# Kernel optimization log

Measured on AMD Instinct MI355X. Metric: run time of the kernel, lower is better.

Reference implementation:

```python
import jax, jax.numpy as jnp
import numpy as np
from jax import lax

# dims: B batch, C=d_model=256, IMG=128, P=4 patch, H=W=32, L=H*W=1024
# D=d_inner=512 (ssm_ratio 2.0), N=d_state=16, R=dt_rank=16, K=4 scan directions
B, C, IMG, P = 2, 256, 128, 4
H = W = IMG // P
L = H * W
D_INNER, N, R, K = 512, 16, 16, 4


def layernorm(x, g, b, eps=1e-5):
    mu = jnp.mean(x, axis=-1, keepdims=True)
    var = jnp.var(x, axis=-1, keepdims=True)
    return (x - mu) * lax.rsqrt(var + eps) * g + b


def setup_inputs() -> dict:
    key = jax.random.key(0)
    ks = jax.random.split(key, 12)
    f = lambda i, shape, s=0.02: jax.random.normal(ks[i], shape, jnp.float32) * s
    A_init = jnp.tile(jnp.arange(1, N + 1, dtype=jnp.float32)[None, None, :], (K, D_INNER, 1))
    return {
        "x": jax.random.normal(ks[0], (B, C, IMG, IMG), jnp.float32),
        "patch_w": f(1, (C, C, P, P)),
        "patch_b": jnp.zeros((C,), jnp.float32),
        "ln_g": jnp.ones((C,), jnp.float32),
        "ln_b": jnp.zeros((C,), jnp.float32),
        "in_w": f(2, (2 * D_INNER, C)),
        "conv_w": f(3, (D_INNER, 1, 3, 3)),
        "conv_b": jnp.zeros((D_INNER,), jnp.float32),
        "xproj_w": f(4, (K, R + 2 * N, D_INNER)),
        "dt_w": f(5, (K, D_INNER, R)),
        "dt_b": f(6, (K, D_INNER), 0.1),
        "A_log": jnp.log(A_init),
        "Ds": jnp.ones((K, D_INNER), jnp.float32),
        "on_g": jnp.ones((D_INNER,), jnp.float32),
        "on_b": jnp.zeros((D_INNER,), jnp.float32),
        "out_w": f(7, (C, D_INNER)),
        "head_w": f(8, (1, C)),
        "head_b": jnp.zeros((1,), jnp.float32),
    }


def _forward(x, patch_w, patch_b, ln_g, ln_b, in_w, conv_w, conv_b, xproj_w,
             dt_w, dt_b, A_log, Ds, on_g, on_b, out_w, head_w, head_b):
    dn = ("NCHW", "OIHW", "NCHW")
    # GRL is identity in forward. Patch embed conv, stride = patch.
    t = lax.conv_general_dilated(x, patch_w, (P, P), "VALID", dimension_numbers=dn)
    t = t + patch_b[None, :, None, None]
    t = jnp.transpose(t, (0, 2, 3, 1))                      # (B,H,W,C)

    # ---- VSS block: t + SS2D(LN(t)) ----
    u = layernorm(t, ln_g, ln_b)
    xz = jnp.einsum("bhwc,ec->bhwe", u, in_w)               # (B,H,W,2D)
    xc, z = jnp.split(xz, 2, axis=-1)
    xc = jnp.transpose(xc, (0, 3, 1, 2))                    # (B,D,H,W)
    xc = lax.conv_general_dilated(xc, conv_w, (1, 1), "SAME",
                                  dimension_numbers=dn, feature_group_count=D_INNER)
    xc = jax.nn.silu(xc + conv_b[None, :, None, None])

    # cross-scan: row-major, col-major, and their reverses -> (B,K,D,L)
    x_hw = xc.reshape(B, D_INNER, L)
    x_wh = jnp.transpose(xc, (0, 1, 3, 2)).reshape(B, D_INNER, L)
    xs = jnp.stack([x_hw, x_wh], axis=1)
    xs = jnp.concatenate([xs, jnp.flip(xs, axis=-1)], axis=1)  # (B,4,D,L)

    x_dbl = jnp.einsum("bkdl,kcd->bkcl", xs, xproj_w)          # (B,K,R+2N,L)
    dts_r = x_dbl[:, :, :R]
    Bs = x_dbl[:, :, R:R + N]                                  # (B,K,N,L)
    Cs = x_dbl[:, :, R + N:]                                   # (B,K,N,L)
    dts = jnp.einsum("bkrl,kdr->bkdl", dts_r, dt_w) + dt_b[None, :, :, None]
    dts = jax.nn.softplus(dts)                                 # (B,K,D,L)

    A = -jnp.exp(A_log)                                        # (K,D,N)
    dA = jnp.exp(dts[:, :, :, None, :] * A[None, :, :, :, None])      # (B,K,D,N,L)
    dBu = (dts * xs)[:, :, :, None, :] * Bs[:, :, None, :, :]         # (B,K,D,N,L)

    dA_t = jnp.moveaxis(dA, -1, 0)        # (L,B,K,D,N)
    dBu_t = jnp.moveaxis(dBu, -1, 0)
    Cs_t = jnp.moveaxis(Cs, -1, 0)        # (L,B,K,N)

    def step(h, inputs):
        dA_i, dBu_i, C_i = inputs
        h = dA_i * h + dBu_i
        y = jnp.einsum("bkdn,bkn->bkd", h, C_i)
        return h, y

    h0 = jnp.zeros((B, K, D_INNER, N), xs.dtype)
    _, ys = lax.scan(step, h0, (dA_t, dBu_t, Cs_t))           # ys: (L,B,K,D)
    ys = jnp.moveaxis(ys, 0, -1)                               # (B,K,D,L)
    ys = ys + Ds[None, :, :, None] * xs

    # cross-merge (invert the 4 scan orders and sum)
    y_rev = jnp.flip(ys[:, 2:], axis=-1)                        # (B,2,D,L)
    y_hw = ys[:, 0] + y_rev[:, 0]
    y_wh = ys[:, 1] + y_rev[:, 1]
    y_wh = jnp.transpose(y_wh.reshape(B, D_INNER, W, H), (0, 1, 3, 2)).reshape(B, D_INNER, L)
    y = (y_hw + y_wh).reshape(B, D_INNER, H, W)
    y = jnp.transpose(y, (0, 2, 3, 1))                          # (B,H,W,D)

    y = layernorm(y, on_g, on_b) * jax.nn.silu(z)
    ss_out = jnp.einsum("bhwd,cd->bhwc", y, out_w)
    t = t + ss_out

    # global average pool + head
    pooled = jnp.mean(t, axis=(1, 2))                           # (B,C)
    return pooled @ head_w.T + head_b


def reference(x, patch_w, patch_b, ln_g, ln_b, in_w, conv_w, conv_b, xproj_w,
              dt_w, dt_b, A_log, Ds, on_g, on_b, out_w, head_w, head_b):
    return _forward(x, patch_w, patch_b, ln_g, ln_b, in_w, conv_w, conv_b, xproj_w,
                    dt_w, dt_b, A_log, Ds, on_g, on_b, out_w, head_w, head_b)
```

## Files before the change

kernel.cpp:

```cpp
#include <hip/hip_runtime.h>
#include <math.h>


typedef __attribute__((ext_vector_type(4))) float f32x4;
typedef __attribute__((ext_vector_type(8))) short bf16x8;

__device__ __forceinline__ ushort bf16_rn(float f) {
  uint u = __float_as_uint(f);
  return (ushort)((u + 0x7fffu + ((u >> 16) & 1u)) >> 16);
}
__device__ __forceinline__ float bf2f(uint us) { return __uint_as_float(us << 16); }
__device__ __forceinline__ uint packbf(float a, float b) {
  return (uint)bf16_rn(a) | ((uint)bf16_rn(b) << 16);
}

__global__ __launch_bounds__(256) void prep_kernel(const float* __restrict__ x,
    ushort* __restrict__ Ap,
    const float* __restrict__ pw, const float* __restrict__ iw,
    const float* __restrict__ ow, const float* __restrict__ xw,
    const float* __restrict__ hw,
    ushort* __restrict__ pwh,
    ushort* __restrict__ iwh, ushort* __restrict__ iwl,
    ushort* __restrict__ xwh, ushort* __restrict__ xwl,
    float* __restrict__ weff) {
  int bid = blockIdx.x;
  int tid = threadIdx.x;
  if (bid < 2048) {
    __shared__ __align__(16) ushort tile[32][136];
    int b = bid >> 10, hh = (bid >> 5) & 31, c0 = (bid & 31) * 8;
    int ci = tid >> 5, ph = (tid >> 3) & 3, w4 = tid & 7;
    const float* src = x + (((long)(b * 256 + c0 + ci) * 128 + 4 * hh + ph) * 128 + 16 * w4);
    #pragma unroll
    for (int j = 0; j < 4; ++j) {
      float4 v = *(const float4*)(src + 4 * j);
      uint2 pk;
      pk.x = packbf(v.x, v.y);
      pk.y = packbf(v.z, v.w);
      *(uint2*)&tile[w4 * 4 + j][ci * 16 + ph * 4] = pk;
    }
    __syncthreads();
    int w = tid >> 3;
    long rowbase = ((long)(b * 1024 + hh * 32 + w)) * 4096 + c0 * 16;
    #pragma unroll
    for (int i = 0; i < 2; ++i) {
      int gr = (tid & 7) + 8 * i;
      *(uint4*)&Ap[rowbase + gr * 8] = *(const uint4*)&tile[w][gr * 8];
    }
  } else {
    int i = (bid - 2048) * 256 + tid;
    if (i < 1048576) {
      pwh[i] = bf16_rn(pw[i]);
      return;
    }
    if (i < 1409024) {
      const float* src; ushort* hi; ushort* lo; int off;
      if (i < 1310720) { src = iw; hi = iwh; lo = iwl; off = i - 1048576; }
      else             { src = xw; hi = xwh; lo = xwl; off = i - 1310720; }
      float f = src[off];
      ushort h = bf16_rn(f);
      hi[off] = h;
      lo[off] = bf16_rn(f - __uint_as_float(((uint)h) << 16));
      return;
    }
    if (i < 1409536) {
      int k = i - 1409024;
      float s = 0.f;
      #pragma unroll 8
      for (int c = 0; c < 256; ++c) s += ow[c * 512 + k] * hw[c];
      weff[k] = s;
    }
  }
}

__global__ __launch_bounds__(512) void mfma_bf(
    const ushort* __restrict__ A, const ushort* __restrict__ Bhi,
    const ushort* __restrict__ Blo, float* __restrict__ Cout, float* __restrict__ C2,
    int M, int N, int K, int kchunk, int mode, int NBM, int NBZ, int uselo)
{
  __shared__ __align__(16) ushort Ah[128 * 64];
  __shared__ __align__(16) ushort Bh[64 * 64];
  __shared__ __align__(16) ushort Bl[64 * 64];
  int tid = threadIdx.x;
  int bid = blockIdx.x;
  int kz = bid % NBZ;
  int n0 = (bid / (NBZ * NBM)) * 64;
  int m0 = ((bid / NBZ) % NBM) * 128;
  int k0 = kz * kchunk;
  int wid = tid >> 6, lane = tid & 63;
  int wm = wid >> 1, wn = wid & 1;
  int lrow = lane & 15, g = lane >> 4;
  f32x4 acc[2][2] = {};
  int nkt = kchunk >> 6;
  for (int kt = 0; kt < nkt; ++kt) {
    int kb = k0 + (kt << 6);
    {
      int gi = tid & 7;
      #pragma unroll
      for (int i = 0; i < 2; ++i) {
        int row = (tid >> 3) + (i << 6);
        uint4 v = *(const uint4*)&A[(long)(m0 + row) * K + kb + gi * 8];
        *(uint4*)&Ah[row * 64 + ((gi ^ (row & 7)) << 3)] = v;
      }
      int row = tid >> 3;
      long off = (long)(n0 + row) * K + kb + gi * 8;
      int la = row * 64 + ((gi ^ (row & 7)) << 3);
      *(uint4*)&Bh[la] = *(const uint4*)&Bhi[off];
      if (uselo) *(uint4*)&Bl[la] = *(const uint4*)&Blo[off];
    }
    __syncthreads();
    #pragma unroll
    for (int kk = 0; kk < 2; ++kk) {
      bf16x8 af[2], bhf[2];
      #pragma unroll
      for (int mi = 0; mi < 2; ++mi) {
        int row = wm * 32 + mi * 16 + lrow;
        af[mi] = *(const bf16x8*)&Ah[row * 64 + ((((kk << 2) + g) ^ (row & 7)) << 3)];
      }
      #pragma unroll
      for (int ni = 0; ni < 2; ++ni) {
        int row = wn * 32 + ni * 16 + lrow;
        int col = (((kk << 2) + g) ^ (row & 7)) << 3;
        bhf[ni] = *(const bf16x8*)&Bh[row * 64 + col];
      }
      #pragma unroll
      for (int mi = 0; mi < 2; ++mi)
        #pragma unroll
        for (int ni = 0; ni < 2; ++ni)
          acc[mi][ni] = __builtin_amdgcn_mfma_f32_16x16x32_bf16(af[mi], bhf[ni], acc[mi][ni], 0, 0, 0);
      if (uselo) {
        #pragma unroll
        for (int ni = 0; ni < 2; ++ni) {
          int row = wn * 32 + ni * 16 + lrow;
          int col = (((kk << 2) + g) ^ (row & 7)) << 3;
          bf16x8 blf = *(const bf16x8*)&Bl[row * 64 + col];
          #pragma unroll
          for (int mi = 0; mi < 2; ++mi)
            acc[mi][ni] = __builtin_amdgcn_mfma_f32_16x16x32_bf16(af[mi], blf, acc[mi][ni], 0, 0, 0);
        }
      }
    }
    __syncthreads();
  }
  int r4 = lane >> 4;
  if (mode == 2) {
    bool xhalf = (n0 < 512);
    ushort* xcb = (ushort*)Cout;
    #pragma unroll
    for (int mi = 0; mi < 2; ++mi)
      #pragma unroll
      for (int ni = 0; ni < 2; ++ni) {
        int n = n0 + wn * 32 + ni * 16 + lrow;
        int mb = m0 + wm * 32 + mi * 16 + r4 * 4;
        int bb = mb >> 10, l = mb & 1023;
        if (xhalf) {
          uint2 o;
          o.x = packbf(acc[mi][ni][0], acc[mi][ni][1]);
          o.y = packbf(acc[mi][ni][2], acc[mi][ni][3]);
          *(uint2*)&xcb[((long)(bb * 512 + n)) * 1024 + l] = o;
        } else {
          #pragma unroll
          for (int r = 0; r < 4; ++r)
            C2[(long)(mb + r) * 512 + (n - 512)] = acc[mi][ni][r];
        }
      }
  } else {
    long zoff = (long)kz * M * N;
    #pragma unroll
    for (int mi = 0; mi < 2; ++mi)
      #pragma unroll
      for (int ni = 0; ni < 2; ++ni) {
        int n = n0 + wn * 32 + ni * 16 + lrow;
        int mb = m0 + wm * 32 + mi * 16 + r4 * 4;
        #pragma unroll
        for (int r = 0; r < 4; ++r)
          Cout[zoff + (long)(mb + r) * N + n] = acc[mi][ni][r];
      }
  }
}

__global__ __launch_bounds__(256) void mfma_x(
    const ushort* __restrict__ A, const ushort* __restrict__ Bhi,
    const ushort* __restrict__ Blo, float* __restrict__ xdbl)
{
  __shared__ __align__(16) ushort Ah[64 * 64];
  __shared__ __align__(16) ushort Bh[48 * 64];
  __shared__ __align__(16) ushort Bl[48 * 64];
  int tid = threadIdx.x;
  int m0 = blockIdx.x * 64;
  int z = blockIdx.y, k = z & 3;
  const ushort* Az = A + (long)z * 524288;
  const ushort* Bhz = Bhi + (long)k * 24576;
  const ushort* Blz = Blo + (long)k * 24576;
  int lane = tid & 63, wv = tid >> 6;
  int lrow = lane & 15, g = lane >> 4;
  f32x4 acc[3] = {};
  for (int kt = 0; kt < 8; ++kt) {
    int kb = kt << 6;
    #pragma unroll
    for (int i = 0; i < 2; ++i) {
      int idx = i * 256 + tid;
      int row = idx >> 3, gi = idx & 7;
      uint4 v = *(const uint4*)&Az[(long)(m0 + row) * 512 + kb + gi * 8];
      *(uint4*)&Ah[row * 64 + ((gi ^ (row & 7)) << 3)] = v;
      if (idx < 384) {
        long off = (long)row * 512 + kb + gi * 8;
        int la = row * 64 + ((gi ^ (row & 7)) << 3);
        *(uint4*)&Bh[la] = *(const uint4*)&Bhz[off];
        *(uint4*)&Bl[la] = *(const uint4*)&Blz[off];
      }
    }
    __syncthreads();
    #pragma unroll
    for (int kk = 0; kk < 2; ++kk) {
      int arow = wv * 16 + lrow;
      bf16x8 af = *(const bf16x8*)&Ah[arow * 64 + ((((kk << 2) + g) ^ (arow & 7)) << 3)];
      #pragma unroll
      for (int ni = 0; ni < 3; ++ni) {
        int brow = ni * 16 + lrow;
        int col = (((kk << 2) + g) ^ (brow & 7)) << 3;
        bf16x8 bh = *(const bf16x8*)&Bh[brow * 64 + col];
        bf16x8 bl = *(const bf16x8*)&Bl[brow * 64 + col];
        acc[ni] = __builtin_amdgcn_mfma_f32_16x16x32_bf16(af, bh, acc[ni], 0, 0, 0);
        acc[ni] = __builtin_amdgcn_mfma_f32_16x16x32_bf16(af, bl, acc[ni], 0, 0, 0);
      }
    }
    __syncthreads();
  }
  float* Cz = xdbl + (long)z * 49152;
  int r4 = lane >> 4;
  #pragma unroll
  for (int ni = 0; ni < 3; ++ni) {
    int n = ni * 16 + lrow;
    int mb = m0 + wv * 16 + r4 * 4;
    #pragma unroll
    for (int r = 0; r < 4; ++r)
      Cz[(long)(mb + r) * 48 + n] = acc[ni][r];
  }
}

__device__ __forceinline__ float blk_sum(float v, float* sm) {
  #pragma unroll
  for (int o = 32; o > 0; o >>= 1) v += __shfl_down(v, o);
  int wid = threadIdx.x >> 6, lane = threadIdx.x & 63;
  __syncthreads();
  if (lane == 0) sm[wid] = v;
  __syncthreads();
  return sm[0] + sm[1] + sm[2] + sm[3];
}
__device__ __forceinline__ void blk_sum2(float& a, float& b, float* sm) {
  #pragma unroll
  for (int o = 32; o > 0; o >>= 1) { a += __shfl_down(a, o); b += __shfl_down(b, o); }
  int wid = threadIdx.x >> 6, lane = threadIdx.x & 63;
  __syncthreads();
  if (lane == 0) { sm[wid * 2] = a; sm[wid * 2 + 1] = b; }
  __syncthreads();
  a = sm[0] + sm[2] + sm[4] + sm[6];
  b = sm[1] + sm[3] + sm[5] + sm[7];
}
__device__ __forceinline__ void blk_sum3(float& a, float& b, float& c, float* sm) {
  #pragma unroll
  for (int o = 32; o > 0; o >>= 1) {
    a += __shfl_down(a, o); b += __shfl_down(b, o); c += __shfl_down(c, o);
  }
  int wid = threadIdx.x >> 6, lane = threadIdx.x & 63;
  __syncthreads();
  if (lane == 0) { sm[wid * 3] = a; sm[wid * 3 + 1] = b; sm[wid * 3 + 2] = c; }
  __syncthreads();
  a = sm[0] + sm[3] + sm[6] + sm[9];
  b = sm[1] + sm[4] + sm[7] + sm[10];
  c = sm[2] + sm[5] + sm[8] + sm[11];
}

__global__ __launch_bounds__(256) void reduce_ln1(const float* __restrict__ P,
    const float* __restrict__ bias, const float* __restrict__ g,
    const float* __restrict__ b, ushort* __restrict__ u,
    const float* __restrict__ hw, float* __restrict__ tpart) {
  __shared__ float sm[12];
  int m = blockIdx.x, c = threadIdx.x;
  float v = bias[c];
  #pragma unroll
  for (int s = 0; s < 4; ++s) v += P[(long)s * 524288 + m * 256 + c];
  float s1 = v, s2 = v * v, s3 = v * hw[c];
  blk_sum3(s1, s2, s3, sm);
  if (c == 0) tpart[m] = s3;
  float mu = s1 * (1.f / 256.f);
  float var = s2 * (1.f / 256.f) - mu * mu;
  float rs = rsqrtf(var + 1e-5f);
  u[(long)m * 256 + c] = bf16_rn((v - mu) * rs * g[c] + b[c]);
}

__global__ __launch_bounds__(256) void head_final(const float* __restrict__ tpart,
    const float* __restrict__ spart, const float* __restrict__ hb,
    float* __restrict__ out) {
  __shared__ float sm[4];
  int b = blockIdx.x, tid = threadIdx.x;
  float s = 0.f;
  #pragma unroll
  for (int j = 0; j < 4; ++j) {
    int m = b * 1024 + tid * 4 + j;
    s += tpart[m] + spart[m];
  }
  float tot = blk_sum(s, sm);
  if (tid == 0) out[b] = tot * (1.f / 1024.f) + hb[0];
}

__global__ __launch_bounds__(256) void dwbuild(const ushort* __restrict__ xc,
    const float* __restrict__ cw, const float* __restrict__ cb,
    ushort* __restrict__ xsTb) {
  __shared__ float pl[3][32][33];
  __shared__ ushort tile[32][34];
  int h = blockIdx.x;
  int d0 = blockIdx.y * 32;
  int z = blockIdx.z;
  int b = z >> 2, k = z & 3;
  int tid = threadIdx.x;
  int dd = tid >> 3, w4 = (tid & 7) * 4;
  #pragma unroll
  for (int r = 0; r < 3; ++r) {
    int hh = h - 1 + r;
    float4 vv = make_float4(0.f, 0.f, 0.f, 0.f);
    if (hh >= 0 && hh < 32) {
      uint2 v = *(const uint2*)&xc[((long)(b * 512 + d0 + dd)) * 1024 + hh * 32 + w4];
      vv.x = bf2f(v.x & 0xffff); vv.y = bf2f(v.x >> 16);
      vv.z = bf2f(v.y & 0xffff); vv.w = bf2f(v.y >> 16);
    }
    pl[r][dd][w4] = vv.x; pl[r][dd][w4 + 1] = vv.y;
    pl[r][dd][w4 + 2] = vv.z; pl[r][dd][w4 + 3] = vv.w;
  }
  float w9[9];
  #pragma unroll
  for (int i = 0; i < 9; ++i) w9[i] = cw[(d0 + dd) * 9 + i];
  float bias = cb[d0 + dd];
  __syncthreads();
  #pragma unroll
  for (int j = 0; j < 4; ++j) {
    int w = w4 + j;
    float acc = 0.f;
    #pragma unroll
    for (int r = 0; r < 3; ++r) {
      if (w > 0)  acc += w9[r * 3 + 0] * pl[r][dd][w - 1];
      acc += w9[r * 3 + 1] * pl[r][dd][w];
      if (w < 31) acc += w9[r * 3 + 2] * pl[r][dd][w + 1];
    }
    acc += bias;
    tile[dd][w] = bf16_rn(acc / (1.f + __expf(-acc)));
  }
  __syncthreads();
  int a = tid >> 5, q = tid & 31;
  #pragma unroll
  for (int i = 0; i < 4; ++i) {
    int w = a + i * 8;
    int r;
    if (k == 0) r = h * 32 + w;
    else if (k == 1) r = w * 32 + h;
    else if (k == 2) r = 1023 - (h * 32 + w);
    else r = 1023 - (w * 32 + h);
    xsTb[((long)z * 1024 + r) * 512 + d0 + q] = tile[q][w];
  }
}

template<bool FINAL>
__global__ __launch_bounds__(128) void scan_chunk6(
    const float* __restrict__ xdbl, ushort* xsb,
    const float* __restrict__ dtw, const float* __restrict__ dtb,
    const float* __restrict__ A_log, const float* __restrict__ Ds,
    float* __restrict__ dsum, float* __restrict__ hpb)
{
  __shared__ float sdt[32][64];
  __shared__ float sxv[16][64];
  __shared__ float sy[16][64];
  __shared__ float sBC[32][32];
  float (*sR)[16] = (float(*)[16])sy;
  int tid = threadIdx.x;
  int dl = tid >> 1, ng = tid & 1;
  int d0 = blockIdx.x * 64;
  int d = d0 + dl;
  int c = blockIdx.y;
  int z = blockIdx.z;
  int k = z & 3;
  long baseD = (long)z * 524288;
  int l0 = c * 32;
  const float* xdz = xdbl + (long)z * 49152 + (long)l0 * 48;
  #pragma unroll
  for (int i = 0; i < 2; ++i) {
    int idx = i * 128 + tid;
    int l = idx >> 3, q = idx & 7;
    *(float4*)&sBC[l][q * 4] = *(const float4*)(xdz + l * 48 + 16 + q * 4);
  }
  {
    int l = tid >> 2, q = tid & 3;
    *(float4*)&sR[l][q * 4] = *(const float4*)(xdz + l * 48 + q * 4);
  }
  float a[8], h[8];
  #pragma unroll
  for (int j = 0; j < 8; ++j) {
    a[j] = -__expf(A_log[((long)k * 512 + d) * 16 + ng * 8 + j]);
    h[j] = 0.f;
  }
  float4 wr0 = *(const float4*)(dtw + ((long)k * 512 + d) * 16);
  float4 wr1 = *(const float4*)(dtw + ((long)k * 512 + d) * 16 + 4);
  float4 wr2 = *(const float4*)(dtw + ((long)k * 512 + d) * 16 + 8);
  float4 wr3 = *(const float4*)(dtw + ((long)k * 512 + d) * 16 + 12);
  float dbias = dtb[k * 512 + d];
  int gbase = c * 65536 + z * 8192 + d * 16 + ng * 8;
  float Dv = 0.f;
  if (FINAL) {
    #pragma unroll
    for (int j = 0; j < 8; ++j) h[j] = hpb[gbase + j];
    Dv = Ds[k * 512 + d];
  }
  __syncthreads();
  #pragma unroll
  for (int li = 0; li < 16; ++li) {
    int l = ng * 16 + li;
    const float* rr = &sR[l][0];
    float acc = dbias;
    acc += wr0.x * rr[0];  acc += wr0.y * rr[1];  acc += wr0.z * rr[2];  acc += wr0.w * rr[3];
    acc += wr1.x * rr[4];  acc += wr1.y * rr[5];  acc += wr1.z * rr[6];  acc += wr1.w * rr[7];
    acc += wr2.x * rr[8];  acc += wr2.y * rr[9];  acc += wr2.z * rr[10]; acc += wr2.w * rr[11];
    acc += wr3.x * rr[12]; acc += wr3.y * rr[13]; acc += wr3.z * rr[14]; acc += wr3.w * rr[15];
    sdt[l][dl] = (acc > 20.f) ? acc : __logf(1.f + __expf(acc));
  }
  __syncthreads();
  int xli = tid >> 3;
  int xdj = (tid & 7) * 8;
  uint4 rxv = *(const uint4*)&xsb[baseD + (long)(l0 + xli) * 512 + d0 + xdj];
  float dtsum = 0.f;
  for (int t = 0; t < 2; ++t) {
    {
      float4 f0, f1;
      f0.x = bf2f(rxv.x & 0xffff); f0.y = bf2f(rxv.x >> 16);
      f0.z = bf2f(rxv.y & 0xffff); f0.w = bf2f(rxv.y >> 16);
      f1.x = bf2f(rxv.z & 0xffff); f1.y = bf2f(rxv.z >> 16);
      f1.z = bf2f(rxv.w & 0xffff); f1.w = bf2f(rxv.w >> 16);
      *(float4*)&sxv[xli][xdj] = f0;
      *(float4*)&sxv[xli][xdj + 4] = f1;
    }
    __syncthreads();
    if (t == 0)
      rxv = *(const uint4*)&xsb[baseD + (long)(l0 + 16 + xli) * 512 + d0 + xdj];
    #pragma unroll
    for (int li = 0; li < 16; ++li) {
      int lr = t * 16 + li;
      float dt = sdt[lr][dl];
      float xv = sxv[li][dl];
      float w = dt * xv;
      float4 B0 = *(const float4*)&sBC[lr][ng * 8];
      float4 B1 = *(const float4*)&sBC[lr][ng * 8 + 4];
      if (!FINAL) {
        dtsum += dt;
        h[0] = __expf(dt * a[0]) * h[0] + w * B0.x;
        h[1] = __expf(dt * a[1]) * h[1] + w * B0.y;
        h[2] = __expf(dt * a[2]) * h[2] + w * B0.z;
        h[3] = __expf(dt * a[3]) * h[3] + w * B0.w;
        h[4] = __expf(dt * a[4]) * h[4] + w * B1.x;
        h[5] = __expf(dt * a[5]) * h[5] + w * B1.y;
        h[6] = __expf(dt * a[6]) * h[6] + w * B1.z;
        h[7] = __expf(dt * a[7]) * h[7] + w * B1.w;
      } else {
        float4 C0 = *(const float4*)&sBC[lr][16 + ng * 8];
        float4 C1 = *(const float4*)&sBC[lr][16 + ng * 8 + 4];
        float p;
        h[0] = __expf(dt * a[0]) * h[0] + w * B0.x; p  = h[0] * C0.x;
        h[1] = __expf(dt * a[1]) * h[1] + w * B0.y; p += h[1] * C0.y;
        h[2] = __expf(dt * a[2]) * h[2] + w * B0.z; p += h[2] * C0.z;
        h[3] = __expf(dt * a[3]) * h[3] + w * B0.w; p += h[3] * C0.w;
        h[4] = __expf(dt * a[4]) * h[4] + w * B1.x; p += h[4] * C1.x;
        h[5] = __expf(dt * a[5]) * h[5] + w * B1.y; p += h[5] * C1.y;
        h[6] = __expf(dt * a[6]) * h[6] + w * B1.z; p += h[6] * C1.z;
        h[7] = __expf(dt * a[7]) * h[7] + w * B1.w; p += h[7] * C1.w;
        p += __shfl_xor(p, 1);
        if (ng == 0) sy[li][dl] = p + Dv * xv;
      }
    }
    __syncthreads();
    if (FINAL) {
      float4 f0 = *(float4*)&sy[xli][xdj];
      float4 f1 = *(float4*)&sy[xli][xdj + 4];
      uint4 o;
      o.x = packbf(f0.x, f0.y); o.y = packbf(f0.z, f0.w);
      o.z = packbf(f1.x, f1.y); o.w = packbf(f1.z, f1.w);
      *(uint4*)&xsb[baseD + (long)(l0 + t * 16 + xli) * 512 + d0 + xdj] = o;
    }
  }
  if (!FINAL) {
    *(float4*)(hpb + gbase)     = make_float4(h[0], h[1], h[2], h[3]);
    *(float4*)(hpb + gbase + 4) = make_float4(h[4], h[5], h[6], h[7]);
    if (ng == 0) dsum[c * 4096 + z * 512 + d] = dtsum;
  }
}

__global__ __launch_bounds__(256) void scan_prefix(const float* __restrict__ dsum,
    const float* __restrict__ A_log, float* __restrict__ hpb) {
  int g = blockIdx.x * 256 + threadIdx.x;
  int z = g >> 13, n = g & 15;
  int d = (g >> 4) & 511;
  int k = z & 3;
  float a = -__expf(A_log[((long)k * 512 + d) * 16 + n]);
  float h = 0.f;
  #pragma unroll
  for (int c = 0; c < 32; ++c) {
    float P = __expf(dsum[c * 4096 + z * 512 + d] * a);
    float hp = hpb[c * 65536 + g];
    hpb[c * 65536 + g] = h;
    h = P * h + hp;
  }
}

__global__ __launch_bounds__(256) void combine_ln2gate(const ushort* __restrict__ ys,
    const float* __restrict__ zb, const float* __restrict__ g,
    const float* __restrict__ b, const float* __restrict__ weff,
    float* __restrict__ spart) {
  __shared__ float sm[8];
  int m = blockIdx.x, tid = threadIdx.x;
  int bb = m >> 10, l = m & 1023;
  int hh = l >> 5, w = l & 31;
  int lw = w * 32 + hh;
  long b4 = (long)bb * 4;
  uint u0 = *(const uint*)&ys[((b4 + 0) * 1024 + l) * 512 + tid * 2];
  uint u1 = *(const uint*)&ys[((b4 + 2) * 1024 + (1023 - l)) * 512 + tid * 2];
  uint u2 = *(const uint*)&ys[((b4 + 1) * 1024 + lw) * 512 + tid * 2];
  uint u3 = *(const uint*)&ys[((b4 + 3) * 1024 + (1023 - lw)) * 512 + tid * 2];
  float v0 = bf2f(u0 & 0xffff) + bf2f(u1 & 0xffff) + bf2f(u2 & 0xffff) + bf2f(u3 & 0xffff);
  float v1 = bf2f(u0 >> 16) + bf2f(u1 >> 16) + bf2f(u2 >> 16) + bf2f(u3 >> 16);
  float s1 = v0 + v1, s2 = v0 * v0 + v1 * v1;
  blk_sum2(s1, s2, sm);
  float mu = s1 * (1.f / 512.f);
  float var = s2 * (1.f / 512.f) - mu * mu;
  float rs = rsqrtf(var + 1e-5f);
  float2 gg = *(const float2*)(g + tid * 2);
  float2 bbv = *(const float2*)(b + tid * 2);
  float2 zz = *(const float2*)(zb + (long)m * 512 + tid * 2);
  float y0 = ((v0 - mu) * rs * gg.x + bbv.x) * (zz.x / (1.f + __expf(-zz.x)));
  float y1 = ((v1 - mu) * rs * gg.y + bbv.y) * (zz.y / (1.f + __expf(-zz.y)));
  float2 we = *(const float2*)(weff + tid * 2);
  float s3 = blk_sum(y0 * we.x + y1 * we.y, sm);
  if (tid == 0) spart[m] = s3;
}

extern "C" void kernel_launch(void* const* d_in, const int* in_sizes, int n_in,
                              void* d_out, int out_size, void* d_ws, size_t ws_size,
                              hipStream_t stream) {
  const float* x       = (const float*)d_in[0];
  const float* patch_w = (const float*)d_in[1];
  const float* patch_b = (const float*)d_in[2];
  const float* ln_g    = (const float*)d_in[3];
  const float* ln_b    = (const float*)d_in[4];
  const float* in_w    = (const float*)d_in[5];
  const float* conv_w  = (const float*)d_in[6];
  const float* conv_b  = (const float*)d_in[7];
  const float* xproj_w = (const float*)d_in[8];
  const float* dt_w    = (const float*)d_in[9];
  const float* dt_b    = (const float*)d_in[10];
  const float* A_log   = (const float*)d_in[11];
  const float* Ds      = (const float*)d_in[12];
  const float* on_g    = (const float*)d_in[13];
  const float* on_b    = (const float*)d_in[14];
  const float* out_w   = (const float*)d_in[15];
  const float* head_w  = (const float*)d_in[16];
  const float* head_b  = (const float*)d_in[17];

  float* ws = (float*)d_ws;
  float*  tpart   = ws;
  float*  spart   = ws + 2048;
  float*  weff_buf= ws + 4096;
  float*  z_buf   = ws + 8192;
  ushort* u_bf    = (ushort*)(ws + 1060864);
  ushort* xc_bf   = (ushort*)(ws + 1323008);
  ushort* xsT_bf  = (ushort*)(ws + 1847296);
  float*  xdbl_buf= ws + 3944448;
  float*  P_patch = ws + 4337664;
  float*  dsum_buf= ws + 6434816;
  float*  hp_buf  = ws + 6565888;
  ushort* A_p     = (ushort*)(ws + 8663040);
  ushort* pw_hi   = (ushort*)(ws + 12857344);
  ushort* iw_hi   = (ushort*)(ws + 13381632);
  ushort* iw_lo   = (ushort*)(ws + 13512704);
  ushort* xw_hi   = (ushort*)(ws + 13643776);
  ushort* xw_lo   = (ushort*)(ws + 13692928);

  prep_kernel<<<7554, 256, 0, stream>>>(x, A_p, patch_w, in_w, out_w, xproj_w,
      head_w, pw_hi, iw_hi, iw_lo, xw_hi, xw_lo, weff_buf);
  mfma_bf<<<256, 512, 0, stream>>>(A_p, pw_hi, nullptr, P_patch, nullptr,
      2048, 256, 4096, 1024, 0, 16, 4, 0);
  reduce_ln1<<<2048, 256, 0, stream>>>(P_patch, patch_b, ln_g, ln_b, u_bf,
      head_w, tpart);
  mfma_bf<<<256, 512, 0, stream>>>(u_bf, iw_hi, iw_lo, (float*)xc_bf, z_buf,
      2048, 1024, 256, 256, 2, 16, 1, 1);
  dwbuild<<<dim3(32, 16, 8), 256, 0, stream>>>(xc_bf, conv_w, conv_b, xsT_bf);
  mfma_x<<<dim3(16, 8), 256, 0, stream>>>(xsT_bf, xw_hi, xw_lo, xdbl_buf);
  scan_chunk6<false><<<dim3(8, 32, 8), 128, 0, stream>>>(xdbl_buf, xsT_bf,
      dt_w, dt_b, A_log, Ds, dsum_buf, hp_buf);
  scan_prefix<<<256, 256, 0, stream>>>(dsum_buf, A_log, hp_buf);
  scan_chunk6<true><<<dim3(8, 32, 8), 128, 0, stream>>>(xdbl_buf, xsT_bf,
      dt_w, dt_b, A_log, Ds, nullptr, hp_buf);
  combine_ln2gate<<<2048, 256, 0, stream>>>(xsT_bf, z_buf, on_g, on_b,
      weff_buf, spart);
  head_final<<<2, 256, 0, stream>>>(tpart, spart, head_b, (float*)d_out);
}
```

Baseline: 133.2 us.

## Fold scan prefix into final chunk pass and split patch GEMM K eight ways

Removes the separate scan_prefix kernel. Each final-pass scan block now recomputes its own incoming state by walking all earlier chunks' carry states and dt sums, which adds redundant work that grows with the chunk index but saves a launch and a serial pass. The patch-embed GEMM split-K goes from 4 to 8 partitions with twice the blocks, reduce_ln1 sums 8 partials, and the workspace offsets are shifted to fit. The xs load is also hoisted earlier so it overlaps with the dt computation.

```diff
diff --git a/kernel.cpp b/kernel.cpp
--- a/kernel.cpp
+++ b/kernel.cpp
@@ -279,7 +279,7 @@
   int m = blockIdx.x, c = threadIdx.x;
   float v = bias[c];
   #pragma unroll
-  for (int s = 0; s < 4; ++s) v += P[(long)s * 524288 + m * 256 + c];
+  for (int s = 0; s < 8; ++s) v += P[(long)s * 524288 + m * 256 + c];
   float s1 = v, s2 = v * v, s3 = v * hw[c];
   blk_sum3(s1, s2, s3, sm);
   if (c == 0) tpart[m] = s3;
@@ -360,7 +360,7 @@
 }
 
 template<bool FINAL>
-__global__ __launch_bounds__(128) void scan_chunk6(
+__global__ __launch_bounds__(128) void scan_chunk7(
     const float* __restrict__ xdbl, ushort* xsb,
     const float* __restrict__ dtw, const float* __restrict__ dtb,
     const float* __restrict__ A_log, const float* __restrict__ Ds,
@@ -391,6 +391,9 @@
     int l = tid >> 2, q = tid & 3;
     *(float4*)&sR[l][q * 4] = *(const float4*)(xdz + l * 48 + q * 4);
   }
+  int xli = tid >> 3;
+  int xdj = (tid & 7) * 8;
+  uint4 rxv = *(const uint4*)&xsb[baseD + (long)(l0 + xli) * 512 + d0 + xdj];
   float a[8], h[8];
   #pragma unroll
   for (int j = 0; j < 8; ++j) {
@@ -402,12 +405,23 @@
   float4 wr2 = *(const float4*)(dtw + ((long)k * 512 + d) * 16 + 8);
   float4 wr3 = *(const float4*)(dtw + ((long)k * 512 + d) * 16 + 12);
   float dbias = dtb[k * 512 + d];
-  int gbase = c * 65536 + z * 8192 + d * 16 + ng * 8;
   float Dv = 0.f;
   if (FINAL) {
-    #pragma unroll
-    for (int j = 0; j < 8; ++j) h[j] = hpb[gbase + j];
     Dv = Ds[k * 512 + d];
+    for (int j = 0; j < c; ++j) {
+      float ds = dsum[j * 4096 + z * 512 + d];
+      int gb = j * 65536 + z * 8192 + d * 16 + ng * 8;
+      float4 hpa = *(const float4*)(hpb + gb);
+      float4 hpbv = *(const float4*)(hpb + gb + 4);
+      h[0] = __expf(ds * a[0]) * h[0] + hpa.x;
+      h[1] = __expf(ds * a[1]) * h[1] + hpa.y;
+      h[2] = __expf(ds * a[2]) * h[2] + hpa.z;
+      h[3] = __expf(ds * a[3]) * h[3] + hpa.w;
+      h[4] = __expf(ds * a[4]) * h[4] + hpbv.x;
+      h[5] = __expf(ds * a[5]) * h[5] + hpbv.y;
+      h[6] = __expf(ds * a[6]) * h[6] + hpbv.z;
+      h[7] = __expf(ds * a[7]) * h[7] + hpbv.w;
+    }
   }
   __syncthreads();
   #pragma unroll
@@ -422,9 +436,6 @@
     sdt[l][dl] = (acc > 20.f) ? acc : __logf(1.f + __expf(acc));
   }
   __syncthreads();
-  int xli = tid >> 3;
-  int xdj = (tid & 7) * 8;
-  uint4 rxv = *(const uint4*)&xsb[baseD + (long)(l0 + xli) * 512 + d0 + xdj];
   float dtsum = 0.f;
   for (int t = 0; t < 2; ++t) {
     {
@@ -484,26 +495,10 @@
     }
   }
   if (!FINAL) {
+    int gbase = c * 65536 + z * 8192 + d * 16 + ng * 8;
     *(float4*)(hpb + gbase)     = make_float4(h[0], h[1], h[2], h[3]);
     *(float4*)(hpb + gbase + 4) = make_float4(h[4], h[5], h[6], h[7]);
     if (ng == 0) dsum[c * 4096 + z * 512 + d] = dtsum;
-  }
-}
-
-__global__ __launch_bounds__(256) void scan_prefix(const float* __restrict__ dsum,
-    const float* __restrict__ A_log, float* __restrict__ hpb) {
-  int g = blockIdx.x * 256 + threadIdx.x;
-  int z = g >> 13, n = g & 15;
-  int d = (g >> 4) & 511;
-  int k = z & 3;
-  float a = -__expf(A_log[((long)k * 512 + d) * 16 + n]);
-  float h = 0.f;
-  #pragma unroll
-  for (int c = 0; c < 32; ++c) {
-    float P = __expf(dsum[c * 4096 + z * 512 + d] * a);
-    float hp = hpb[c * 65536 + g];
-    hpb[c * 65536 + g] = h;
-    h = P * h + hp;
   }
 }
 
@@ -565,35 +560,34 @@
   float*  spart   = ws + 2048;
   float*  weff_buf= ws + 4096;
   float*  z_buf   = ws + 8192;
-  ushort* u_bf    = (ushort*)(ws + 1060864);
-  ushort* xc_bf   = (ushort*)(ws + 1323008);
-  ushort* xsT_bf  = (ushort*)(ws + 1847296);
-  float*  xdbl_buf= ws + 3944448;
-  float*  P_patch = ws + 4337664;
-  float*  dsum_buf= ws + 6434816;
-  float*  hp_buf  = ws + 6565888;
-  ushort* A_p     = (ushort*)(ws + 8663040);
-  ushort* pw_hi   = (ushort*)(ws + 12857344);
-  ushort* iw_hi   = (ushort*)(ws + 13381632);
-  ushort* iw_lo   = (ushort*)(ws + 13512704);
-  ushort* xw_hi   = (ushort*)(ws + 13643776);
-  ushort* xw_lo   = (ushort*)(ws + 13692928);
+  ushort* u_bf    = (ushort*)(ws + 1056768);
+  ushort* xc_bf   = (ushort*)(ws + 1318912);
+  ushort* xsT_bf  = (ushort*)(ws + 1843200);
+  float*  xdbl_buf= ws + 3940352;
+  float*  P_patch = ws + 4333568;
+  float*  dsum_buf= ws + 8527872;
+  float*  hp_buf  = ws + 8658944;
+  ushort* A_p     = (ushort*)(ws + 10756096);
+  ushort* pw_hi   = (ushort*)(ws + 14950400);
+  ushort* iw_hi   = (ushort*)(ws + 15474688);
+  ushort* iw_lo   = (ushort*)(ws + 15605760);
+  ushort* xw_hi   = (ushort*)(ws + 15736832);
+  ushort* xw_lo   = (ushort*)(ws + 15785984);
 
   prep_kernel<<<7554, 256, 0, stream>>>(x, A_p, patch_w, in_w, out_w, xproj_w,
       head_w, pw_hi, iw_hi, iw_lo, xw_hi, xw_lo, weff_buf);
-  mfma_bf<<<256, 512, 0, stream>>>(A_p, pw_hi, nullptr, P_patch, nullptr,
-      2048, 256, 4096, 1024, 0, 16, 4, 0);
+  mfma_bf<<<512, 512, 0, stream>>>(A_p, pw_hi, nullptr, P_patch, nullptr,
+      2048, 256, 4096, 512, 0, 16, 8, 0);
   reduce_ln1<<<2048, 256, 0, stream>>>(P_patch, patch_b, ln_g, ln_b, u_bf,
       head_w, tpart);
   mfma_bf<<<256, 512, 0, stream>>>(u_bf, iw_hi, iw_lo, (float*)xc_bf, z_buf,
       2048, 1024, 256, 256, 2, 16, 1, 1);
   dwbuild<<<dim3(32, 16, 8), 256, 0, stream>>>(xc_bf, conv_w, conv_b, xsT_bf);
   mfma_x<<<dim3(16, 8), 256, 0, stream>>>(xsT_bf, xw_hi, xw_lo, xdbl_buf);
-  scan_chunk6<false><<<dim3(8, 32, 8), 128, 0, stream>>>(xdbl_buf, xsT_bf,
+  scan_chunk7<false><<<dim3(8, 32, 8), 128, 0, stream>>>(xdbl_buf, xsT_bf,
       dt_w, dt_b, A_log, Ds, dsum_buf, hp_buf);
-  scan_prefix<<<256, 256, 0, stream>>>(dsum_buf, A_log, hp_buf);
-  scan_chunk6<true><<<dim3(8, 32, 8), 128, 0, stream>>>(xdbl_buf, xsT_bf,
-      dt_w, dt_b, A_log, Ds, nullptr, hp_buf);
+  scan_chunk7<true><<<dim3(8, 32, 8), 128, 0, stream>>>(xdbl_buf, xsT_bf,
+      dt_w, dt_b, A_log, Ds, dsum_buf, hp_buf);
   combine_ln2gate<<<2048, 256, 0, stream>>>(xsT_bf, z_buf, on_g, on_b,
       weff_buf, spart);
   head_final<<<2, 256, 0, stream>>>(tpart, spart, head_b, (float*)d_out);
```

After: 136.9 us. 2.8% more time.
